# Optimization experiments

Hardware: AMD Instinct MI355X
Metric: run time of the kernel (lower is better)

Reference implementation:

```python
import jax, jax.numpy as jnp
import numpy as np

N = 50000
E = 1600000
SI, SO, VI, VO, H, SVOD = 128, 128, 16, 16, 16, 3
EPS = 1e-8


def _safe_norm(x, axis, keepdims=False):
    return jnp.sqrt(jnp.sum(x * x, axis=axis, keepdims=keepdims) + EPS)


def setup_inputs() -> dict:
    key = jax.random.key(0)
    ks = jax.random.split(key, 13)

    def lin(k, fan_in, shape):
        b = 1.0 / np.sqrt(fan_in)
        return jax.random.uniform(k, shape, jnp.float32, -b, b)

    merged_dim = H + SI + 3 * SVOD  # 153
    return {
        "s": jax.random.normal(ks[0], (N, SI), jnp.float32),
        "v": jax.random.normal(ks[1], (N, VI, 3), jnp.float32),
        "frames": jax.random.normal(ks[2], (E, 3, 3), jnp.float32),
        "W_vd": lin(ks[3], VI, (VI, H)),            # vector_down (no bias)
        "W_vdf": lin(ks[4], VI, (VI, SVOD)),        # vector_down_frames (no bias)
        "W_so": lin(ks[5], merged_dim, (merged_dim, SO)),  # scalar_out
        "b_so": lin(ks[6], merged_dim, (SO,)),
        "W_vu": lin(ks[7], H, (H, VO)),             # vector_up (no bias)
        "W_vosf": lin(ks[8], SO, (SO, 3 * SVOD)),   # vector_out_scale_frames
        "b_vosf": lin(ks[9], SO, (3 * SVOD,)),
        "W_vuf": lin(ks[10], SVOD, (SVOD, VO)),     # vector_up_frames (no bias)
        "edge_index": jax.random.randint(ks[11], (2, E), 0, N, jnp.int32),
        "node_inputs": 1,
    }


def reference(s, v, frames, W_vd, W_vdf, W_so, b_so, W_vu, W_vosf, b_vosf, W_vuf, edge_index, node_inputs):
    # node_inputs is assumed truthy (node-wise GCP): gather by source node, scatter-mean back.
    row = edge_index[0]
    deg = jax.ops.segment_sum(jnp.ones((E,), s.dtype), row, num_segments=N)
    inv_deg = 1.0 / jnp.maximum(deg, 1.0)

    v_pre = jnp.swapaxes(v, -1, -2)                 # [N, 3, VI]
    vh = v_pre @ W_vd                                # [N, 3, H]
    vnorm = _safe_norm(vh, axis=-2)                  # [N, H]
    vdf = v_pre @ W_vdf                              # [N, 3, SVOD]

    # scalarize: project gathered source-node vectors onto per-edge frames, scatter-mean
    local = jnp.einsum('eij,ejc->eic', frames, vdf[row])       # [E, 3, SVOD]
    local9 = jnp.swapaxes(local, -1, -2).reshape(E, 3 * SVOD)  # [E, 9]
    sh = jax.ops.segment_sum(local9, row, num_segments=N) * inv_deg[:, None]  # [N, 9]

    merged = jnp.concatenate([s, vnorm, sh], axis=-1)          # [N, SI+H+9]
    scalar_rep = merged @ W_so + b_so                           # [N, SO]

    # vector path with frame gate
    vr = jnp.swapaxes(vh @ W_vu, -1, -2)                        # [N, VO, 3]
    gate = jax.nn.sigmoid(scalar_rep) @ W_vosf + b_vosf         # [N, 9]
    # vectorize: expand gate scalars back into vectors via frames, scatter-mean
    g = gate[row].reshape(E, 3, 3)
    gv_e = jnp.einsum('eji,ejk->eik', g, frames)                # [E, 3, 3]
    gv = jax.ops.segment_sum(gv_e, row, num_segments=N) * inv_deg[:, None, None]  # [N, 3, 3]
    gvr = jnp.swapaxes(jnp.swapaxes(gv, -1, -2) @ W_vuf, -1, -2)  # [N, VO, 3]
    vr = vr * jax.nn.sigmoid(_safe_norm(gvr, axis=-1, keepdims=True))

    return jax.nn.relu(scalar_rep), vr
```

## Files before the change

### kernel.cpp

```cpp
#include <hip/hip_runtime.h>

#define N_NODES 50000
#define N_EDGES 1600000
#define NPB     16
#define NCHAIN  16
#define KSTR    168
#define EPSV    1e-8f

typedef float f32x4 __attribute__((ext_vector_type(4)));
typedef short s16x8 __attribute__((ext_vector_type(8)));

struct f4u { float a, b, c, d; };

__device__ __forceinline__ float sigmoidf_(float x) { return 1.0f / (1.0f + __expf(-x)); }
__device__ __forceinline__ short f2bf(float x) {
    unsigned u = __float_as_uint(x);
    unsigned r = (u + 0x7FFFu + ((u >> 16) & 1u)) >> 16;
    return (short)r;
}
__device__ __forceinline__ float bf2f(short h) {
    return __uint_as_float(((unsigned)(unsigned short)h) << 16);
}

__global__ __launch_bounds__(256) void init_kernel(
    const float* __restrict__ W_so, short* __restrict__ WThi, short* __restrict__ WTlo,
    int* __restrict__ head) {
    int i = blockIdx.x * 256 + threadIdx.x;
    if (i < 128 * 160) {
        int o = i / 160, k = i - o * 160;
        float w = (k < 153) ? W_so[k * 128 + o] : 0.0f;
        short hh = f2bf(w);
        WThi[i] = hh;
        WTlo[i] = f2bf(w - bf2f(hh));
    }
    if (i < N_NODES * NCHAIN) head[i] = -1;
}

__global__ __launch_bounds__(256) void bucket_kernel(
    const int* __restrict__ row,
    int* __restrict__ head,
    int* __restrict__ nxt) {
    int e = blockIdx.x * 256 + threadIdx.x;
    if (e >= N_EDGES) return;
    int r = row[e];
    int prev = atomicExch(&head[r * NCHAIN + (e & (NCHAIN - 1))], e);
    nxt[e] = prev;
}

__global__ __launch_bounds__(256, 8) void node_kernel(
    const float* __restrict__ s,
    const float* __restrict__ v,
    const float* __restrict__ frames,
    const float* __restrict__ W_vd,
    const float* __restrict__ W_vdf,
    const short* __restrict__ WThi,
    const short* __restrict__ WTlo,
    const float* __restrict__ b_so,
    const float* __restrict__ W_vu,
    const float* __restrict__ W_vosf,
    const float* __restrict__ b_vosf,
    const float* __restrict__ W_vuf,
    const int* __restrict__ head,
    const int* __restrict__ nxt,
    float* __restrict__ out0,
    float* __restrict__ out1)
{
    __shared__ __align__(16) short AL[2][NPB][KSTR];
    __shared__ float vL[NPB][48];
    __shared__ float vhL[NPB][3][16];
    __shared__ float FbarL[NPB][9];
    __shared__ float vdfL[NPB][9];
    __shared__ float gateL[NPB][12];

    float (*sigL)[128] = (float (*)[128])&AL[0][0][0];

    const int t = threadIdx.x;
    const int base = blockIdx.x * NPB;
    const int nn = t >> 4, h = t & 15;
    const int n = base + nn;

    int e = head[(size_t)n * NCHAIN + h];

#pragma unroll
    for (int r = 0; r < 3; r++) vL[nn][h * 3 + r] = v[(size_t)n * 48 + h * 3 + r];
    {
        const float4* sp4 = (const float4*)(s + (size_t)n * 128 + h * 8);
        float4 s0 = sp4[0], s1 = sp4[1];
        float sv[8] = {s0.x, s0.y, s0.z, s0.w, s1.x, s1.y, s1.z, s1.w};
        s16x8 shi, slo;
#pragma unroll
        for (int j = 0; j < 8; j++) {
            short hh = f2bf(sv[j]);
            shi[j] = hh;
            slo[j] = f2bf(sv[j] - bf2f(hh));
        }
        *(s16x8*)&AL[0][nn][h * 8] = shi;
        *(s16x8*)&AL[1][nn][h * 8] = slo;
    }

    {
        float fs[10];
#pragma unroll
        for (int k = 0; k < 10; k++) fs[k] = 0.f;
        while (e >= 0) {
            int en = nxt[e];
            const float* f = frames + (size_t)e * 9;
            const f4u* fp = (const f4u*)f;
            f4u x = fp[0];
            f4u y = fp[1];
            float z8 = f[8];
            fs[0] += x.a; fs[1] += x.b; fs[2] += x.c; fs[3] += x.d;
            fs[4] += y.a; fs[5] += y.b; fs[6] += y.c; fs[7] += y.d;
            fs[8] += z8;
            fs[9] += 1.0f;
            e = en;
        }
#pragma unroll
        for (int m = 1; m < 16; m <<= 1) {
#pragma unroll
            for (int k = 0; k < 10; k++) fs[k] += __shfl_xor(fs[k], m);
        }
        if (h < 9) {
            float inv = 1.0f / fmaxf(fs[9], 1.0f);
            FbarL[nn][h] = fs[h] * inv;
        }
    }
    __syncthreads();

    {
        float vh0 = 0.f, vh1 = 0.f, vh2 = 0.f;
#pragma unroll
        for (int i = 0; i < 16; i++) {
            float w = W_vd[i * 16 + h];
            vh0 += vL[nn][i * 3 + 0] * w;
            vh1 += vL[nn][i * 3 + 1] * w;
            vh2 += vL[nn][i * 3 + 2] * w;
        }
        vhL[nn][0][h] = vh0; vhL[nn][1][h] = vh1; vhL[nn][2][h] = vh2;
        float vn = sqrtf(vh0 * vh0 + vh1 * vh1 + vh2 * vh2 + EPSV);
        short hh = f2bf(vn);
        AL[0][nn][128 + h] = hh;
        AL[1][nn][128 + h] = f2bf(vn - bf2f(hh));
        if (h < 3) {
            int cc = h;
#pragma unroll
            for (int j = 0; j < 3; j++) {
                float a = 0.f;
#pragma unroll
                for (int i = 0; i < 16; i++) a += vL[nn][i * 3 + j] * W_vdf[i * 3 + cc];
                vdfL[nn][j * 3 + cc] = a;
            }
        }
    }
    __syncthreads();

    {
        if (h < 9) {
            int c = h / 3, i = h % 3;
            float a = 0.f;
#pragma unroll
            for (int j = 0; j < 3; j++) a += FbarL[nn][i * 3 + j] * vdfL[nn][j * 3 + c];
            short hh = f2bf(a);
            AL[0][nn][144 + h] = hh;
            AL[1][nn][144 + h] = f2bf(a - bf2f(hh));
        } else {
            AL[0][nn][144 + h] = 0;
            AL[1][nn][144 + h] = 0;
        }
    }
    __syncthreads();

    {
        const int w = t >> 6;
        const int lane = t & 63;
        const int quad = lane >> 4;
        const int col = lane & 15;
        const int o0 = w * 32 + col, o1 = o0 + 16;
        f32x4 acc0 = (f32x4){0.f, 0.f, 0.f, 0.f};
        f32x4 acc1 = (f32x4){0.f, 0.f, 0.f, 0.f};
#pragma unroll
        for (int kk = 0; kk < 5; kk++) {
            const int krow = kk * 32 + quad * 8;
            s16x8 ahi = *(const s16x8*)&AL[0][col][krow];
            s16x8 alo = *(const s16x8*)&AL[1][col][krow];
            s16x8 b0h = *(const s16x8*)&WThi[o0 * 160 + krow];
            s16x8 b0l = *(const s16x8*)&WTlo[o0 * 160 + krow];
            s16x8 b1h = *(const s16x8*)&WThi[o1 * 160 + krow];
            s16x8 b1l = *(const s16x8*)&WTlo[o1 * 160 + krow];
            acc0 = __builtin_amdgcn_mfma_f32_16x16x32_bf16(ahi, b0h, acc0, 0, 0, 0);
            acc0 = __builtin_amdgcn_mfma_f32_16x16x32_bf16(ahi, b0l, acc0, 0, 0, 0);
            acc0 = __builtin_amdgcn_mfma_f32_16x16x32_bf16(alo, b0h, acc0, 0, 0, 0);
            acc1 = __builtin_amdgcn_mfma_f32_16x16x32_bf16(ahi, b1h, acc1, 0, 0, 0);
            acc1 = __builtin_amdgcn_mfma_f32_16x16x32_bf16(ahi, b1l, acc1, 0, 0, 0);
            acc1 = __builtin_amdgcn_mfma_f32_16x16x32_bf16(alo, b1h, acc1, 0, 0, 0);
        }
        __syncthreads();
        {
            float b0 = b_so[o0], b1 = b_so[o1];
#pragma unroll
            for (int r = 0; r < 4; r++) {
                int nl = quad * 4 + r;
                float v0 = acc0[r] + b0;
                float v1 = acc1[r] + b1;
                out0[(size_t)(base + nl) * 128 + o0] = fmaxf(v0, 0.0f);
                out0[(size_t)(base + nl) * 128 + o1] = fmaxf(v1, 0.0f);
                sigL[nl][o0] = sigmoidf_(v0);
                sigL[nl][o1] = sigmoidf_(v1);
            }
        }
    }
    __syncthreads();

    {
        const float* sp = &sigL[nn][h * 8];
        float4 s0 = *(const float4*)sp;
        float4 s1 = *(const float4*)(sp + 4);
        float sv[8] = {s0.x, s0.y, s0.z, s0.w, s1.x, s1.y, s1.z, s1.w};
        float p[9];
#pragma unroll
        for (int k = 0; k < 9; k++) p[k] = 0.f;
#pragma unroll
        for (int i = 0; i < 8; i++) {
            int o = h * 8 + i;
#pragma unroll
            for (int k = 0; k < 9; k++) p[k] += sv[i] * W_vosf[o * 9 + k];
        }
#pragma unroll
        for (int m = 1; m < 16; m <<= 1) {
#pragma unroll
            for (int k = 0; k < 9; k++) p[k] += __shfl_xor(p[k], m);
        }
        if (h < 9) gateL[nn][h] = p[h] + b_vosf[h];
    }
    __syncthreads();

    {
        int o = h;
        float gv[9];
#pragma unroll
        for (int i = 0; i < 3; i++)
#pragma unroll
            for (int kk = 0; kk < 3; kk++) {
                float a = 0.f;
#pragma unroll
                for (int j = 0; j < 3; j++) a += gateL[nn][j * 3 + i] * FbarL[nn][j * 3 + kk];
                gv[i * 3 + kk] = a;
            }
        float gvr[3];
#pragma unroll
        for (int kk = 0; kk < 3; kk++) {
            float a = 0.f;
#pragma unroll
            for (int i = 0; i < 3; i++) a += gv[i * 3 + kk] * W_vuf[i * 16 + o];
            gvr[kk] = a;
        }
        float gn2 = sqrtf(gvr[0] * gvr[0] + gvr[1] * gvr[1] + gvr[2] * gvr[2] + EPSV);
        float sg = sigmoidf_(gn2);
#pragma unroll
        for (int c = 0; c < 3; c++) {
            float a = 0.f;
#pragma unroll
            for (int h2 = 0; h2 < 16; h2++) a += vhL[nn][c][h2] * W_vu[h2 * 16 + o];
            out1[(size_t)n * 48 + o * 3 + c] = a * sg;
        }
    }
}

extern "C" void kernel_launch(void* const* d_in, const int* in_sizes, int n_in,
                              void* d_out, int out_size, void* d_ws, size_t ws_size,
                              hipStream_t stream) {
    const float* s      = (const float*)d_in[0];
    const float* v      = (const float*)d_in[1];
    const float* frames = (const float*)d_in[2];
    const float* W_vd   = (const float*)d_in[3];
    const float* W_vdf  = (const float*)d_in[4];
    const float* W_so   = (const float*)d_in[5];
    const float* b_so   = (const float*)d_in[6];
    const float* W_vu   = (const float*)d_in[7];
    const float* W_vosf = (const float*)d_in[8];
    const float* b_vosf = (const float*)d_in[9];
    const float* W_vuf  = (const float*)d_in[10];
    const int* edge_index = (const int*)d_in[11];

    const size_t head_b = (size_t)N_NODES * NCHAIN * sizeof(int);
    const size_t next_b = (size_t)N_EDGES * sizeof(int);
    int*   head = (int*)d_ws;
    int*   nxt  = (int*)((char*)d_ws + head_b);
    short* WThi = (short*)((char*)d_ws + head_b + next_b);
    short* WTlo = WThi + 128 * 160;
    float* out0 = (float*)d_out;
    float* out1 = out0 + (size_t)N_NODES * 128;

    init_kernel<<<(N_NODES * NCHAIN + 255) / 256, 256, 0, stream>>>(W_so, WThi, WTlo, head);
    bucket_kernel<<<(N_EDGES + 255) / 256, 256, 0, stream>>>(edge_index, head, nxt);
    node_kernel<<<N_NODES / NPB, 256, 0, stream>>>(
        s, v, frames, W_vd, W_vdf, WThi, WTlo, b_so, W_vu, W_vosf, b_vosf, W_vuf,
        head, nxt, out0, out1);
}
```

Before: 294.5 us.

## Pack per-edge frames and next pointer into 64-byte payload during bucketing

```diff
diff --git a/kernel.cpp b/kernel.cpp
--- a/kernel.cpp
+++ b/kernel.cpp
@@ -36,7 +36,28 @@
     if (i < N_NODES * NCHAIN) head[i] = -1;
 }
 
-__global__ __launch_bounds__(256) void bucket_kernel(
+__global__ __launch_bounds__(256) void bucket_fat_kernel(
+    const int* __restrict__ row,
+    const float* __restrict__ frames,
+    int* __restrict__ head,
+    float* __restrict__ pay) {
+    int e = blockIdx.x * 256 + threadIdx.x;
+    if (e >= N_EDGES) return;
+    int r = row[e];
+    int prev = atomicExch(&head[r * NCHAIN + (e & (NCHAIN - 1))], e);
+    const float* f = frames + (size_t)e * 9;
+    const f4u* fp = (const f4u*)f;
+    f4u x = fp[0];
+    f4u y = fp[1];
+    float z8 = f[8];
+    float4* dst = (float4*)(pay + (size_t)e * 16);
+    dst[0] = make_float4(x.a, x.b, x.c, x.d);
+    dst[1] = make_float4(y.a, y.b, y.c, y.d);
+    dst[2] = make_float4(z8, __int_as_float(prev), 0.0f, 0.0f);
+    dst[3] = make_float4(0.0f, 0.0f, 0.0f, 0.0f);
+}
+
+__global__ __launch_bounds__(256) void bucket_thin_kernel(
     const int* __restrict__ row,
     int* __restrict__ head,
     int* __restrict__ nxt) {
@@ -47,10 +68,11 @@
     nxt[e] = prev;
 }
 
-__global__ __launch_bounds__(256, 8) void node_kernel(
+template<int FAT>
+__global__ __launch_bounds__(256) void node_kernel(
     const float* __restrict__ s,
     const float* __restrict__ v,
-    const float* __restrict__ frames,
+    const float* __restrict__ fr,
     const float* __restrict__ W_vd,
     const float* __restrict__ W_vdf,
     const short* __restrict__ WThi,
@@ -102,18 +124,33 @@
         float fs[10];
 #pragma unroll
         for (int k = 0; k < 10; k++) fs[k] = 0.f;
-        while (e >= 0) {
-            int en = nxt[e];
-            const float* f = frames + (size_t)e * 9;
-            const f4u* fp = (const f4u*)f;
-            f4u x = fp[0];
-            f4u y = fp[1];
-            float z8 = f[8];
-            fs[0] += x.a; fs[1] += x.b; fs[2] += x.c; fs[3] += x.d;
-            fs[4] += y.a; fs[5] += y.b; fs[6] += y.c; fs[7] += y.d;
-            fs[8] += z8;
-            fs[9] += 1.0f;
-            e = en;
+        if (FAT) {
+            while (e >= 0) {
+                const float4* p = (const float4*)(fr + (size_t)e * 16);
+                float4 c2 = p[2];
+                float4 c0 = p[0];
+                float4 c1 = p[1];
+                int en = __float_as_int(c2.y);
+                fs[0] += c0.x; fs[1] += c0.y; fs[2] += c0.z; fs[3] += c0.w;
+                fs[4] += c1.x; fs[5] += c1.y; fs[6] += c1.z; fs[7] += c1.w;
+                fs[8] += c2.x;
+                fs[9] += 1.0f;
+                e = en;
+            }
+        } else {
+            while (e >= 0) {
+                int en = nxt[e];
+                const float* f = fr + (size_t)e * 9;
+                const f4u* fp = (const f4u*)f;
+                f4u x = fp[0];
+                f4u y = fp[1];
+                float z8 = f[8];
+                fs[0] += x.a; fs[1] += x.b; fs[2] += x.c; fs[3] += x.d;
+                fs[4] += y.a; fs[5] += y.b; fs[6] += y.c; fs[7] += y.d;
+                fs[8] += z8;
+                fs[9] += 1.0f;
+                e = en;
+            }
         }
 #pragma unroll
         for (int m = 1; m < 16; m <<= 1) {
@@ -283,17 +320,28 @@
     const int* edge_index = (const int*)d_in[11];
 
     const size_t head_b = (size_t)N_NODES * NCHAIN * sizeof(int);
-    const size_t next_b = (size_t)N_EDGES * sizeof(int);
+    const size_t wt_b   = (size_t)128 * 160 * sizeof(short);
+    const size_t pay_off = head_b + 2 * wt_b;
     int*   head = (int*)d_ws;
-    int*   nxt  = (int*)((char*)d_ws + head_b);
-    short* WThi = (short*)((char*)d_ws + head_b + next_b);
+    short* WThi = (short*)((char*)d_ws + head_b);
     short* WTlo = WThi + 128 * 160;
     float* out0 = (float*)d_out;
     float* out1 = out0 + (size_t)N_NODES * 128;
 
+    const size_t fat_need = pay_off + (size_t)N_EDGES * 64;
     init_kernel<<<(N_NODES * NCHAIN + 255) / 256, 256, 0, stream>>>(W_so, WThi, WTlo, head);
-    bucket_kernel<<<(N_EDGES + 255) / 256, 256, 0, stream>>>(edge_index, head, nxt);
-    node_kernel<<<N_NODES / NPB, 256, 0, stream>>>(
-        s, v, frames, W_vd, W_vdf, WThi, WTlo, b_so, W_vu, W_vosf, b_vosf, W_vuf,
-        head, nxt, out0, out1);
-}
+
+    if (ws_size >= fat_need) {
+        float* pay = (float*)((char*)d_ws + pay_off);
+        bucket_fat_kernel<<<(N_EDGES + 255) / 256, 256, 0, stream>>>(edge_index, frames, head, pay);
+        node_kernel<1><<<N_NODES / NPB, 256, 0, stream>>>(
+            s, v, pay, W_vd, W_vdf, WThi, WTlo, b_so, W_vu, W_vosf, b_vosf, W_vuf,
+            head, (const int*)nullptr, out0, out1);
+    } else {
+        int* nxt = (int*)((char*)d_ws + pay_off);
+        bucket_thin_kernel<<<(N_EDGES + 255) / 256, 256, 0, stream>>>(edge_index, head, nxt);
+        node_kernel<0><<<N_NODES / NPB, 256, 0, stream>>>(
+            s, v, frames, W_vd, W_vdf, WThi, WTlo, b_so, W_vu, W_vosf, b_vosf, W_vuf,
+            head, nxt, out0, out1);
+    }
+}
```

Result: no change. 292.6 us (-0.6%).
